# Performance work log

Hardware: AMD Instinct MI355X
Metric: run time of the kernel (lower is better)

## Reference

```python
import jax, jax.numpy as jnp
import numpy as np

STRIDE, PAD, DIL, DG = 1, 1, 1, 1
KH, KW = 3, 3


def setup_inputs() -> dict:
    key = jax.random.key(0)
    k1, k2, k3 = jax.random.split(key, 3)
    B, Cin, H, W, Cout = 8, 128, 64, 64, 256
    Ho = (H + 2 * PAD - (DIL * (KH - 1) + 1)) // STRIDE + 1
    Wo = (W + 2 * PAD - (DIL * (KW - 1) + 1)) // STRIDE + 1
    x = jax.random.normal(k1, (B, Cin, H, W), jnp.float32)
    offset = jax.random.normal(k2, (B, DG * 2 * KH * KW, Ho, Wo), jnp.float32)
    stdv = 1.0 / np.sqrt(Cin * KH * KW)
    weight = jax.random.uniform(k3, (Cout, Cin, KH, KW), jnp.float32, -stdv, stdv)
    return {"x": x, "offset": offset, "weight": weight}


def deform_conv2d(x, offset, weight, stride=STRIDE, pad=PAD, dil=DIL, dg=DG):
    """Deformable conv v1: per-tap learned offsets + bilinear gather + GEMM."""
    B, C, H, W = x.shape
    Co, Ci, kh, kw = weight.shape
    K = kh * kw
    cg = C // dg  # channels per deformable group
    Ho = (H + 2 * pad - (dil * (kh - 1) + 1)) // stride + 1
    Wo = (W + 2 * pad - (dil * (kw - 1) + 1)) // stride + 1

    # offset layout: [B, dg*K*2, Ho, Wo] with (dy, dx) interleaved per tap
    off = offset.reshape(B, dg, K, 2, Ho, Wo)

    # base sampling positions per output pixel and kernel tap
    ky, kx = jnp.meshgrid(jnp.arange(kh), jnp.arange(kw), indexing="ij")
    base_y = (jnp.arange(Ho) * stride - pad)[None, :, None] + (ky.reshape(K) * dil)[:, None, None]  # [K,Ho,1]
    base_x = (jnp.arange(Wo) * stride - pad)[None, None, :] + (kx.reshape(K) * dil)[:, None, None]  # [K,1,Wo]

    py = base_y[None, None].astype(offset.dtype) + off[:, :, :, 0]  # [B,dg,K,Ho,Wo]
    px = base_x[None, None].astype(offset.dtype) + off[:, :, :, 1]  # [B,dg,K,Ho,Wo]

    y0f = jnp.floor(py)
    x0f = jnp.floor(px)
    fy = py - y0f
    fx = px - x0f
    y0 = y0f.astype(jnp.int32)
    x0 = x0f.astype(jnp.int32)
    y1 = y0 + 1
    x1 = x0 + 1

    x_flat = x.reshape(B, dg, cg, H * W)

    def corner(yi, xi, w):
        # zero out contributions whose corner falls outside the image
        valid = (yi >= 0) & (yi < H) & (xi >= 0) & (xi < W)
        idx = jnp.clip(yi, 0, H - 1) * W + jnp.clip(xi, 0, W - 1)  # [B,dg,K,Ho,Wo]
        g = jax.vmap(jax.vmap(lambda xf, i: xf[:, i]))(x_flat, idx)  # [B,dg,cg,K,Ho,Wo]
        return g * (w * valid)[:, :, None]

    cols = (corner(y0, x0, (1 - fy) * (1 - fx))
            + corner(y0, x1, (1 - fy) * fx)
            + corner(y1, x0, fy * (1 - fx))
            + corner(y1, x1, fy * fx))  # [B,dg,cg,K,Ho,Wo]

    w_r = weight.reshape(Co, dg, cg, K)
    return jnp.einsum("bgckhw,ogck->bohw", cols, w_r)


def reference(x, offset, weight):
    return deform_conv2d(x, offset, weight)
```

## Files before the change

kernel.cpp:

```cpp
#include <hip/hip_runtime.h>
#include <hip/hip_bf16.h>

#define CIN   128
#define HH    64
#define WW    64
#define COUT  256
#define HO    64
#define WO    64
#define NTAP  9
#define KTOT  (CIN*NTAP)
#define BK    32
#define NSTEP (KTOT/BK)
#define NB    8
#define PXB   32
#define CROW  272

typedef __attribute__((ext_vector_type(8))) short bf16x8;
typedef __attribute__((ext_vector_type(4))) short bf16x4;
typedef __attribute__((ext_vector_type(4))) float f32x4;

struct __align__(16) TapEntry {
  int   i00, i01, i10, i11;
  float w00, w01, w10, w11;
};

static __device__ __forceinline__ ushort f2bf(float v) {
  unsigned u = __float_as_uint(v);
  unsigned rnd = 0x7fffu + ((u >> 16) & 1u);
  return (ushort)((u + rnd) >> 16);
}
static __device__ __forceinline__ float bf2f(short s) {
  return __uint_as_float(((unsigned)(unsigned short)s) << 16);
}

__global__ __launch_bounds__(256) void prep(const float* __restrict__ x,
                                            const float* __restrict__ w,
                                            ushort* __restrict__ xt,
                                            ushort* __restrict__ wbt) {
  const int blk = blockIdx.x;
  const int tid = threadIdx.x;
  if (blk < NB * HH) {
    const int b = blk >> 6, y = blk & 63;
    const int px = tid & 63, c8 = tid >> 6;
    const float* src = x + (size_t)b * CIN * HH * WW + y * WW + px;
    ushort* dst = xt + (((size_t)(b * HH + y) * WW) + px) * CIN;
    #pragma unroll
    for (int cc = 0; cc < 4; ++cc) {
      const int c0 = cc * 32 + c8 * 8;
      bf16x8 v;
      #pragma unroll
      for (int j = 0; j < 8; ++j)
        v[j] = (short)f2bf(src[(size_t)(c0 + j) * (HH * WW)]);
      *reinterpret_cast<bf16x8*>(dst + c0) = v;
    }
  } else {
    const int h = (blk - NB * HH) * 256 + tid;
    const int s   = h >> 10;
    const int c16 = (h >> 6) & 15;
    const int l   = h & 63;
    const int q   = l >> 4;
    const int r   = l & 15;
    const int co  = c16 * 16 + r;
    const int tap = s >> 2;
    const int ci0 = (s & 3) * 32 + q * 8;
    bf16x8 o;
    #pragma unroll
    for (int j = 0; j < 8; ++j)
      o[j] = (short)f2bf(w[(size_t)(co * CIN + ci0 + j) * NTAP + tap]);
    *reinterpret_cast<bf16x8*>(wbt + (size_t)h * 8) = o;
  }
}

__global__ __launch_bounds__(256, 4)
void dcn8(const ushort* __restrict__ xt, const float* __restrict__ off,
          const ushort* __restrict__ wbt, float* __restrict__ out)
{
  __shared__ TapEntry taps[NTAP * PXB];
  __shared__ __align__(16) char colsB[PXB * CROW];

  const int tid = threadIdx.x;
  const int b  = blockIdx.x & 7;
  const int ho = (blockIdx.x >> 3) & 63;
  const int ph = blockIdx.x >> 9;

  for (int e = tid; e < NTAP * PXB; e += 256) {
    const int k  = e >> 5;
    const int lw = e & 31;
    const int wo = ph * PXB + lw;
    const float* op = off + (((size_t)(b * 18 + 2 * k) * HO + ho) * WO + wo);
    const float dy = op[0];
    const float dx = op[HO * WO];
    const float py  = (float)(ho - 1 + (k / 3)) + dy;
    const float pxf = (float)(wo - 1 + (k % 3)) + dx;
    const float y0f = floorf(py), x0f = floorf(pxf);
    const float fy = py - y0f, fx = pxf - x0f;
    const int y0 = (int)y0f, x0 = (int)x0f;
    const int y1 = y0 + 1,  x1 = x0 + 1;
    const bool vy0 = (unsigned)y0 < HH, vy1 = (unsigned)y1 < HH;
    const bool vx0 = (unsigned)x0 < WW, vx1 = (unsigned)x1 < WW;
    const int cy0 = min(max(y0, 0), HH - 1), cy1 = min(max(y1, 0), HH - 1);
    const int cx0 = min(max(x0, 0), WW - 1), cx1 = min(max(x1, 0), WW - 1);
    TapEntry t;
    t.i00 = (cy0 * WW + cx0) << 8;  t.i01 = (cy0 * WW + cx1) << 8;
    t.i10 = (cy1 * WW + cx0) << 8;  t.i11 = (cy1 * WW + cx1) << 8;
    const float gy = 1.f - fy, gx = 1.f - fx;
    t.w00 = (vy0 && vx0) ? gy * gx : 0.f;
    t.w01 = (vy0 && vx1) ? gy * fx : 0.f;
    t.w10 = (vy1 && vx0) ? fy * gx : 0.f;
    t.w11 = (vy1 && vx1) ? fy * fx : 0.f;
    taps[e] = t;
  }

  const int lane = tid & 63;
  const int grp  = tid >> 6;
  const int l15  = lane & 15;
  const int q    = lane >> 4;
  const int s16b = l15 * 16;

  f32x4 acc[4][2];
  #pragma unroll
  for (int m = 0; m < 4; ++m)
    #pragma unroll
    for (int n = 0; n < 2; ++n)
      acc[m][n] = 0.f;

  const char* xb = reinterpret_cast<const char*>(xt)
                 + (size_t)b * (HH * WW * CIN * 2) + s16b;

  __syncthreads();

  #pragma unroll 1
  for (int tap = 0; tap < NTAP; ++tap) {
    const int px0 = (grp << 3) + q;
    const int px1 = (grp << 3) + 4 + q;
    const TapEntry te0 = taps[tap * PXB + px0];
    const TapEntry te1 = taps[tap * PXB + px1];
    const bf16x8 a00 = *reinterpret_cast<const bf16x8*>(xb + te0.i00);
    const bf16x8 a01 = *reinterpret_cast<const bf16x8*>(xb + te0.i01);
    const bf16x8 a10 = *reinterpret_cast<const bf16x8*>(xb + te0.i10);
    const bf16x8 a11 = *reinterpret_cast<const bf16x8*>(xb + te0.i11);
    const bf16x8 b00 = *reinterpret_cast<const bf16x8*>(xb + te1.i00);
    const bf16x8 b01 = *reinterpret_cast<const bf16x8*>(xb + te1.i01);
    const bf16x8 b10 = *reinterpret_cast<const bf16x8*>(xb + te1.i10);
    const bf16x8 b11 = *reinterpret_cast<const bf16x8*>(xb + te1.i11);
    bf16x8 h0, h1;
    #pragma unroll
    for (int j = 0; j < 8; ++j) {
      const float v0 = te0.w00 * bf2f(a00[j]) + te0.w01 * bf2f(a01[j])
                     + te0.w10 * bf2f(a10[j]) + te0.w11 * bf2f(a11[j]);
      h0[j] = (short)f2bf(v0);
      const float v1 = te1.w00 * bf2f(b00[j]) + te1.w01 * bf2f(b01[j])
                     + te1.w10 * bf2f(b10[j]) + te1.w11 * bf2f(b11[j]);
      h1[j] = (short)f2bf(v1);
    }

    __syncthreads();

    *reinterpret_cast<bf16x8*>(colsB + px0 * CROW + s16b) = h0;
    *reinterpret_cast<bf16x8*>(colsB + px1 * CROW + s16b) = h1;

    __syncthreads();

    #pragma unroll
    for (int kk = 0; kk < 4; ++kk) {
      const int s = tap * 4 + kk;
      bf16x8 a[4], bb[2];
      #pragma unroll
      for (int m = 0; m < 4; ++m)
        a[m] = *reinterpret_cast<const bf16x8*>(
            wbt + ((size_t)((s * 16 + grp * 4 + m) * 64 + lane)) * 8);
      #pragma unroll
      for (int n = 0; n < 2; ++n)
        bb[n] = *reinterpret_cast<const bf16x8*>(
            colsB + (n * 16 + l15) * CROW + kk * 64 + q * 16);
      #pragma unroll
      for (int m = 0; m < 4; ++m)
        #pragma unroll
        for (int n = 0; n < 2; ++n)
          acc[m][n] = __builtin_amdgcn_mfma_f32_16x16x32_bf16(
              a[m], bb[n], acc[m][n], 0, 0, 0);
    }
  }

  #pragma unroll
  for (int m = 0; m < 4; ++m)
    #pragma unroll
    for (int n = 0; n < 2; ++n)
      #pragma unroll
      for (int r = 0; r < 4; ++r) {
        const int co = grp * 64 + m * 16 + q * 4 + r;
        const int wo = ph * PXB + n * 16 + l15;
        out[(((size_t)b * COUT + co) * HO + ho) * WO + wo] = acc[m][n][r];
      }
}

__global__ __launch_bounds__(256, 2)
void dcn_f32(const float* __restrict__ x, const float* __restrict__ off,
             const float* __restrict__ wgt, float* __restrict__ out)
{
  __shared__ TapEntry taps[NTAP * WO];
  __shared__ __align__(16) ushort colsf[WO * 40];
  const int tid = threadIdx.x;
  const int b  = blockIdx.x & 7;
  const int ho = blockIdx.x >> 3;
  for (int e = tid; e < NTAP * WO; e += 256) {
    const int k  = e >> 6;
    const int wo = e & 63;
    const float* op = off + (((size_t)(b * 18 + 2 * k) * HO + ho) * WO + wo);
    const float dy = op[0];
    const float dx = op[HO * WO];
    const float py  = (float)(ho - 1 + (k / 3)) + dy;
    const float pxf = (float)(wo - 1 + (k % 3)) + dx;
    const float y0f = floorf(py), x0f = floorf(pxf);
    const float fy = py - y0f, fx = pxf - x0f;
    const int y0 = (int)y0f, x0 = (int)x0f;
    const int y1 = y0 + 1,  x1 = x0 + 1;
    const bool vy0 = (unsigned)y0 < HH, vy1 = (unsigned)y1 < HH;
    const bool vx0 = (unsigned)x0 < WW, vx1 = (unsigned)x1 < WW;
    const int cy0 = min(max(y0, 0), HH - 1), cy1 = min(max(y1, 0), HH - 1);
    const int cx0 = min(max(x0, 0), WW - 1), cx1 = min(max(x1, 0), WW - 1);
    TapEntry t;
    t.i00 = cy0 * WW + cx0; t.i01 = cy0 * WW + cx1;
    t.i10 = cy1 * WW + cx0; t.i11 = cy1 * WW + cx1;
    const float gy = 1.f - fy, gx = 1.f - fx;
    t.w00 = (vy0 && vx0) ? gy * gx : 0.f;
    t.w01 = (vy0 && vx1) ? gy * fx : 0.f;
    t.w10 = (vy1 && vx0) ? fy * gx : 0.f;
    t.w11 = (vy1 && vx1) ? fy * fx : 0.f;
    taps[e] = t;
  }
  const int px = tid & 63, grp = tid >> 6, lane = tid & 63;
  const int l15 = lane & 15, q = lane >> 4;
  f32x4 acc[4][4];
  #pragma unroll
  for (int m = 0; m < 4; ++m)
    #pragma unroll
    for (int n = 0; n < 4; ++n) acc[m][n] = 0.f;
  const float* xb = x + (size_t)b * CIN * HH * WW;
  __syncthreads();
  for (int tap = 0; tap < NTAP; ++tap) {
    const TapEntry e = taps[tap * WO + px];
    for (int cb = 0; cb < 4; ++cb) {
      __syncthreads();
      {
        const float* xp = xb + (size_t)(cb * 32 + grp * 8) * (HH * WW);
        bf16x8 hv;
        #pragma unroll
        for (int j = 0; j < 8; ++j) {
          const float* p = xp + j * (HH * WW);
          const float v = e.w00 * p[e.i00] + e.w01 * p[e.i01]
                        + e.w10 * p[e.i10] + e.w11 * p[e.i11];
          hv[j] = (short)f2bf(v);
        }
        *reinterpret_cast<bf16x8*>(
            reinterpret_cast<char*>(colsf) + px * 80 + grp * 16) = hv;
      }
      __syncthreads();
      bf16x8 a[4], bbf[4];
      #pragma unroll
      for (int m = 0; m < 4; ++m) {
        const int co = grp * 64 + m * 16 + l15;
        bf16x8 t;
        #pragma unroll
        for (int j = 0; j < 8; ++j)
          t[j] = (short)f2bf(wgt[(size_t)(co * CIN + cb * 32 + q * 8 + j) * NTAP + tap]);
        a[m] = t;
      }
      #pragma unroll
      for (int n = 0; n < 4; ++n)
        bbf[n] = *reinterpret_cast<const bf16x8*>(
            reinterpret_cast<const char*>(colsf) + (n * 16 + l15) * 80 + q * 16);
      #pragma unroll
      for (int m = 0; m < 4; ++m)
        #pragma unroll
        for (int n = 0; n < 4; ++n)
          acc[m][n] = __builtin_amdgcn_mfma_f32_16x16x32_bf16(
              a[m], bbf[n], acc[m][n], 0, 0, 0);
    }
  }
  const int wco = grp * 64;
  #pragma unroll
  for (int m = 0; m < 4; ++m)
    #pragma unroll
    for (int n = 0; n < 4; ++n)
      #pragma unroll
      for (int r = 0; r < 4; ++r) {
        const int co = wco + m * 16 + q * 4 + r;
        const int wo = n * 16 + l15;
        out[(((size_t)b * COUT + co) * HO + ho) * WO + wo] = acc[m][n][r];
      }
}

extern "C" void kernel_launch(void* const* d_in, const int* in_sizes, int n_in,
                              void* d_out, int out_size, void* d_ws, size_t ws_size,
                              hipStream_t stream) {
  const float* x   = (const float*)d_in[0];
  const float* off = (const float*)d_in[1];
  const float* wgt = (const float*)d_in[2];
  float* out = (float*)d_out;

  const size_t xt_bytes = (size_t)NB * HH * WW * CIN * sizeof(ushort);
  const size_t wb_bytes = (size_t)NSTEP * COUT * BK * sizeof(ushort);
  if (ws_size >= xt_bytes + wb_bytes) {
    ushort* xtp  = (ushort*)d_ws;
    ushort* wbtp = (ushort*)((char*)d_ws + xt_bytes);
    const int wchunks = NSTEP * COUT * BK / 8;
    const int wblocks = wchunks / 256;
    prep<<<NB * HH + wblocks, 256, 0, stream>>>(x, wgt, xtp, wbtp);
    dcn8<<<NB * HO * 2, 256, 0, stream>>>(xtp, off, wbtp, out);
  } else {
    dcn_f32<<<NB * HO, 256, 0, stream>>>(x, off, wgt, out);
  }
}
```

Before: 51.05 us.

## Double-buffer bilinear column tile and prefetch next tap's gathers during MFMA

The column tile in shared memory is now double-buffered. The gather loads for tap+1 are issued before the MFMA loop of the current tap, and the bilinear combine is written to the other buffer afterwards, so global gather latency overlaps with matrix math and one barrier per tap is removed. The bilinear combine is also rewritten with packed f32x2 math and a v_cvt_pk_bf16_f32 instruction in place of the scalar rounding routine. This costs more registers for the in-flight gathers and twice the LDS for the column tile, which could reduce occupancy.

```diff
diff --git a/kernel.cpp b/kernel.cpp
--- a/kernel.cpp
+++ b/kernel.cpp
@@ -14,10 +14,13 @@
 #define NB    8
 #define PXB   32
 #define CROW  272
+#define CBUF  (PXB*CROW)
 
 typedef __attribute__((ext_vector_type(8))) short bf16x8;
 typedef __attribute__((ext_vector_type(4))) short bf16x4;
 typedef __attribute__((ext_vector_type(4))) float f32x4;
+typedef __attribute__((ext_vector_type(2))) float f32x2;
+typedef __attribute__((ext_vector_type(4))) unsigned int u32x4;
 
 struct __align__(16) TapEntry {
   int   i00, i01, i10, i11;
@@ -31,6 +34,31 @@
 }
 static __device__ __forceinline__ float bf2f(short s) {
   return __uint_as_float(((unsigned)(unsigned short)s) << 16);
+}
+static __device__ __forceinline__ f32x2 unpack2(unsigned dw) {
+  f32x2 r;
+  r.x = __uint_as_float(dw << 16);
+  r.y = __uint_as_float(dw & 0xffff0000u);
+  return r;
+}
+
+static __device__ __forceinline__ u32x4 combine_pk(const u32x4 c00, const u32x4 c01,
+                                                   const u32x4 c10, const u32x4 c11,
+                                                   const float w00, const float w01,
+                                                   const float w10, const float w11) {
+  u32x4 out;
+  #pragma unroll
+  for (int d = 0; d < 4; ++d) {
+    f32x2 a;
+    a  = unpack2(c00[d]) * f32x2{w00, w00};
+    a += unpack2(c01[d]) * f32x2{w01, w01};
+    a += unpack2(c10[d]) * f32x2{w10, w10};
+    a += unpack2(c11[d]) * f32x2{w11, w11};
+    unsigned r;
+    asm("v_cvt_pk_bf16_f32 %0, %1, %2" : "=v"(r) : "v"(a.x), "v"(a.y));
+    out[d] = r;
+  }
+  return out;
 }
 
 __global__ __launch_bounds__(256) void prep(const float* __restrict__ x,
@@ -72,11 +100,11 @@
 }
 
 __global__ __launch_bounds__(256, 4)
-void dcn8(const ushort* __restrict__ xt, const float* __restrict__ off,
+void dcn9(const ushort* __restrict__ xt, const float* __restrict__ off,
           const ushort* __restrict__ wbt, float* __restrict__ out)
 {
   __shared__ TapEntry taps[NTAP * PXB];
-  __shared__ __align__(16) char colsB[PXB * CROW];
+  __shared__ __align__(16) char colsB[2 * CBUF];
 
   const int tid = threadIdx.x;
   const int b  = blockIdx.x & 7;
@@ -116,6 +144,8 @@
   const int l15  = lane & 15;
   const int q    = lane >> 4;
   const int s16b = l15 * 16;
+  const int px0  = (grp << 3) + q;
+  const int px1  = (grp << 3) + 4 + q;
 
   f32x4 acc[4][2];
   #pragma unroll
@@ -129,37 +159,47 @@
 
   __syncthreads();
 
+  {
+    const TapEntry t0 = taps[px0];
+    const TapEntry t1 = taps[px1];
+    const u32x4 a00 = *reinterpret_cast<const u32x4*>(xb + t0.i00);
+    const u32x4 a01 = *reinterpret_cast<const u32x4*>(xb + t0.i01);
+    const u32x4 a10 = *reinterpret_cast<const u32x4*>(xb + t0.i10);
+    const u32x4 a11 = *reinterpret_cast<const u32x4*>(xb + t0.i11);
+    const u32x4 b00 = *reinterpret_cast<const u32x4*>(xb + t1.i00);
+    const u32x4 b01 = *reinterpret_cast<const u32x4*>(xb + t1.i01);
+    const u32x4 b10 = *reinterpret_cast<const u32x4*>(xb + t1.i10);
+    const u32x4 b11 = *reinterpret_cast<const u32x4*>(xb + t1.i11);
+    const u32x4 h0 = combine_pk(a00, a01, a10, a11, t0.w00, t0.w01, t0.w10, t0.w11);
+    const u32x4 h1 = combine_pk(b00, b01, b10, b11, t1.w00, t1.w01, t1.w10, t1.w11);
+    *reinterpret_cast<u32x4*>(colsB + px0 * CROW + s16b) = h0;
+    *reinterpret_cast<u32x4*>(colsB + px1 * CROW + s16b) = h1;
+  }
+  __syncthreads();
+
   #pragma unroll 1
   for (int tap = 0; tap < NTAP; ++tap) {
-    const int px0 = (grp << 3) + q;
-    const int px1 = (grp << 3) + 4 + q;
-    const TapEntry te0 = taps[tap * PXB + px0];
-    const TapEntry te1 = taps[tap * PXB + px1];
-    const bf16x8 a00 = *reinterpret_cast<const bf16x8*>(xb + te0.i00);
-    const bf16x8 a01 = *reinterpret_cast<const bf16x8*>(xb + te0.i01);
-    const bf16x8 a10 = *reinterpret_cast<const bf16x8*>(xb + te0.i10);
-    const bf16x8 a11 = *reinterpret_cast<const bf16x8*>(xb + te0.i11);
-    const bf16x8 b00 = *reinterpret_cast<const bf16x8*>(xb + te1.i00);
-    const bf16x8 b01 = *reinterpret_cast<const bf16x8*>(xb + te1.i01);
-    const bf16x8 b10 = *reinterpret_cast<const bf16x8*>(xb + te1.i10);
-    const bf16x8 b11 = *reinterpret_cast<const bf16x8*>(xb + te1.i11);
-    bf16x8 h0, h1;
-    #pragma unroll
-    for (int j = 0; j < 8; ++j) {
-      const float v0 = te0.w00 * bf2f(a00[j]) + te0.w01 * bf2f(a01[j])
-                     + te0.w10 * bf2f(a10[j]) + te0.w11 * bf2f(a11[j]);
-      h0[j] = (short)f2bf(v0);
-      const float v1 = te1.w00 * bf2f(b00[j]) + te1.w01 * bf2f(b01[j])
-                     + te1.w10 * bf2f(b10[j]) + te1.w11 * bf2f(b11[j]);
-      h1[j] = (short)f2bf(v1);
-    }
-
-    __syncthreads();
-
-    *reinterpret_cast<bf16x8*>(colsB + px0 * CROW + s16b) = h0;
-    *reinterpret_cast<bf16x8*>(colsB + px1 * CROW + s16b) = h1;
-
-    __syncthreads();
+    const int  cur  = tap & 1;
+    const char* rbuf = colsB + cur * CBUF;
+    char*       wbuf = colsB + (cur ^ 1) * CBUF;
+    const bool  more = (tap + 1) < NTAP;
+
+    u32x4 a00, a01, a10, a11, b00, b01, b10, b11;
+    float w0a, w1a, w2a, w3a, w0b, w1b, w2b, w3b;
+    if (more) {
+      const TapEntry t0 = taps[(tap + 1) * PXB + px0];
+      const TapEntry t1 = taps[(tap + 1) * PXB + px1];
+      a00 = *reinterpret_cast<const u32x4*>(xb + t0.i00);
+      a01 = *reinterpret_cast<const u32x4*>(xb + t0.i01);
+      a10 = *reinterpret_cast<const u32x4*>(xb + t0.i10);
+      a11 = *reinterpret_cast<const u32x4*>(xb + t0.i11);
+      b00 = *reinterpret_cast<const u32x4*>(xb + t1.i00);
+      b01 = *reinterpret_cast<const u32x4*>(xb + t1.i01);
+      b10 = *reinterpret_cast<const u32x4*>(xb + t1.i10);
+      b11 = *reinterpret_cast<const u32x4*>(xb + t1.i11);
+      w0a = t0.w00; w1a = t0.w01; w2a = t0.w10; w3a = t0.w11;
+      w0b = t1.w00; w1b = t1.w01; w2b = t1.w10; w3b = t1.w11;
+    }
 
     #pragma unroll
     for (int kk = 0; kk < 4; ++kk) {
@@ -172,7 +212,7 @@
       #pragma unroll
       for (int n = 0; n < 2; ++n)
         bb[n] = *reinterpret_cast<const bf16x8*>(
-            colsB + (n * 16 + l15) * CROW + kk * 64 + q * 16);
+            rbuf + (n * 16 + l15) * CROW + kk * 64 + q * 16);
       #pragma unroll
       for (int m = 0; m < 4; ++m)
         #pragma unroll
@@ -180,6 +220,14 @@
           acc[m][n] = __builtin_amdgcn_mfma_f32_16x16x32_bf16(
               a[m], bb[n], acc[m][n], 0, 0, 0);
     }
+
+    if (more) {
+      const u32x4 h0 = combine_pk(a00, a01, a10, a11, w0a, w1a, w2a, w3a);
+      const u32x4 h1 = combine_pk(b00, b01, b10, b11, w0b, w1b, w2b, w3b);
+      *reinterpret_cast<u32x4*>(wbuf + px0 * CROW + s16b) = h0;
+      *reinterpret_cast<u32x4*>(wbuf + px1 * CROW + s16b) = h1;
+    }
+    __syncthreads();
   }
 
   #pragma unroll
@@ -307,7 +355,7 @@
     const int wchunks = NSTEP * COUT * BK / 8;
     const int wblocks = wchunks / 256;
     prep<<<NB * HH + wblocks, 256, 0, stream>>>(x, wgt, xtp, wbtp);
-    dcn8<<<NB * HO * 2, 256, 0, stream>>>(xtp, off, wbtp, out);
+    dcn9<<<NB * HO * 2, 256, 0, stream>>>(xtp, off, wbtp, out);
   } else {
     dcn_f32<<<NB * HO, 256, 0, stream>>>(x, off, wgt, out);
   }
```

Result: slower. 71.02 us (+39.1%).

## Process full output row per block with 512 threads and 32-channel warp tiles

Applied to the files above, without the earlier changes.

Merges the two half-row blocks into a single 512-thread block that covers all 64 output pixels of a row. Each of the 8 waves now owns 32 output channels across all 64 pixels instead of 64 channels across 32 pixels. The weight fragments loaded from global memory are shared across more pixels, which halves redundant weight traffic per output. The costs are a doubled shared-memory footprint, half as many blocks for scheduling, and more LDS reads of the column tile per wave.

```diff
diff --git a/kernel.cpp b/kernel.cpp
--- a/kernel.cpp
+++ b/kernel.cpp
@@ -12,7 +12,6 @@
 #define BK    32
 #define NSTEP (KTOT/BK)
 #define NB    8
-#define PXB   32
 #define CROW  272
 
 typedef __attribute__((ext_vector_type(8))) short bf16x8;
@@ -71,22 +70,20 @@
   }
 }
 
-__global__ __launch_bounds__(256, 4)
-void dcn8(const ushort* __restrict__ xt, const float* __restrict__ off,
-          const ushort* __restrict__ wbt, float* __restrict__ out)
+__global__ __launch_bounds__(512, 4)
+void dcn11(const ushort* __restrict__ xt, const float* __restrict__ off,
+           const ushort* __restrict__ wbt, float* __restrict__ out)
 {
-  __shared__ TapEntry taps[NTAP * PXB];
-  __shared__ __align__(16) char colsB[PXB * CROW];
+  __shared__ TapEntry taps[NTAP * WO];
+  __shared__ __align__(16) char colsB[WO * CROW];
 
   const int tid = threadIdx.x;
   const int b  = blockIdx.x & 7;
-  const int ho = (blockIdx.x >> 3) & 63;
-  const int ph = blockIdx.x >> 9;
-
-  for (int e = tid; e < NTAP * PXB; e += 256) {
-    const int k  = e >> 5;
-    const int lw = e & 31;
-    const int wo = ph * PXB + lw;
+  const int ho = blockIdx.x >> 3;
+
+  for (int e = tid; e < NTAP * WO; e += 512) {
+    const int k  = e >> 6;
+    const int wo = e & 63;
     const float* op = off + (((size_t)(b * 18 + 2 * k) * HO + ho) * WO + wo);
     const float dy = op[0];
     const float dx = op[HO * WO];
@@ -111,17 +108,19 @@
     taps[e] = t;
   }
 
+  const int wv   = tid >> 6;
   const int lane = tid & 63;
-  const int grp  = tid >> 6;
   const int l15  = lane & 15;
   const int q    = lane >> 4;
   const int s16b = l15 * 16;
-
-  f32x4 acc[4][2];
+  const int px0  = (wv << 3) + q;
+  const int px1  = (wv << 3) + 4 + q;
+
+  f32x4 acc[2][4];
   #pragma unroll
-  for (int m = 0; m < 4; ++m)
-    #pragma unroll
-    for (int n = 0; n < 2; ++n)
+  for (int m = 0; m < 2; ++m)
+    #pragma unroll
+    for (int n = 0; n < 4; ++n)
       acc[m][n] = 0.f;
 
   const char* xb = reinterpret_cast<const char*>(xt)
@@ -131,10 +130,8 @@
 
   #pragma unroll 1
   for (int tap = 0; tap < NTAP; ++tap) {
-    const int px0 = (grp << 3) + q;
-    const int px1 = (grp << 3) + 4 + q;
-    const TapEntry te0 = taps[tap * PXB + px0];
-    const TapEntry te1 = taps[tap * PXB + px1];
+    const TapEntry te0 = taps[tap * WO + px0];
+    const TapEntry te1 = taps[tap * WO + px1];
     const bf16x8 a00 = *reinterpret_cast<const bf16x8*>(xb + te0.i00);
     const bf16x8 a01 = *reinterpret_cast<const bf16x8*>(xb + te0.i01);
     const bf16x8 a10 = *reinterpret_cast<const bf16x8*>(xb + te0.i10);
@@ -164,32 +161,32 @@
     #pragma unroll
     for (int kk = 0; kk < 4; ++kk) {
       const int s = tap * 4 + kk;
-      bf16x8 a[4], bb[2];
-      #pragma unroll
-      for (int m = 0; m < 4; ++m)
+      bf16x8 a[2], bb[4];
+      #pragma unroll
+      for (int m = 0; m < 2; ++m)
         a[m] = *reinterpret_cast<const bf16x8*>(
-            wbt + ((size_t)((s * 16 + grp * 4 + m) * 64 + lane)) * 8);
-      #pragma unroll
-      for (int n = 0; n < 2; ++n)
+            wbt + ((size_t)((s * 16 + wv * 2 + m) * 64 + lane)) * 8);
+      #pragma unroll
+      for (int n = 0; n < 4; ++n)
         bb[n] = *reinterpret_cast<const bf16x8*>(
             colsB + (n * 16 + l15) * CROW + kk * 64 + q * 16);
       #pragma unroll
-      for (int m = 0; m < 4; ++m)
+      for (int m = 0; m < 2; ++m)
         #pragma unroll
-        for (int n = 0; n < 2; ++n)
+        for (int n = 0; n < 4; ++n)
           acc[m][n] = __builtin_amdgcn_mfma_f32_16x16x32_bf16(
               a[m], bb[n], acc[m][n], 0, 0, 0);
     }
   }
 
   #pragma unroll
-  for (int m = 0; m < 4; ++m)
-    #pragma unroll
-    for (int n = 0; n < 2; ++n)
+  for (int m = 0; m < 2; ++m)
+    #pragma unroll
+    for (int n = 0; n < 4; ++n)
       #pragma unroll
       for (int r = 0; r < 4; ++r) {
-        const int co = grp * 64 + m * 16 + q * 4 + r;
-        const int wo = ph * PXB + n * 16 + l15;
+        const int co = wv * 32 + m * 16 + q * 4 + r;
+        const int wo = n * 16 + l15;
         out[(((size_t)b * COUT + co) * HO + ho) * WO + wo] = acc[m][n][r];
       }
 }
@@ -307,7 +304,7 @@
     const int wchunks = NSTEP * COUT * BK / 8;
     const int wblocks = wchunks / 256;
     prep<<<NB * HH + wblocks, 256, 0, stream>>>(x, wgt, xtp, wbtp);
-    dcn8<<<NB * HO * 2, 256, 0, stream>>>(xtp, off, wbtp, out);
+    dcn11<<<NB * HO, 512, 0, stream>>>(xtp, off, wbtp, out);
   } else {
     dcn_f32<<<NB * HO, 256, 0, stream>>>(x, off, wgt, out);
   }
```

After: 57.24 us. +12.1%, slower.

## Prefetch bilinear corner gathers into LDS via global_load_lds one tap ahead

Applied to the files above, without the earlier changes.

Replaces the direct global loads of the four bilinear corners with asynchronous global-to-LDS loads into a per-wave staging buffer. The loads for the next tap are issued after the current tap's corners are consumed, so the gather latency overlaps the MFMA GEMM of the current tap. This adds 32KB of shared memory per block and lowers the launch-bounds occupancy hint from 4 to 2 blocks, which may reduce latency hiding across waves. The staging buffer is single-buffered, which relies on the vmcnt/lgkmcnt waits to keep reads and new writes ordered.

```diff
diff --git a/kernel.cpp b/kernel.cpp
--- a/kernel.cpp
+++ b/kernel.cpp
@@ -31,6 +31,12 @@
 }
 static __device__ __forceinline__ float bf2f(short s) {
   return __uint_as_float(((unsigned)(unsigned short)s) << 16);
+}
+
+static __device__ __forceinline__ void gload_lds16(const char* g, char* l) {
+  __builtin_amdgcn_global_load_lds(
+      (const __attribute__((address_space(1))) unsigned int*)g,
+      (__attribute__((address_space(3))) unsigned int*)l, 16, 0, 0);
 }
 
 __global__ __launch_bounds__(256) void prep(const float* __restrict__ x,
@@ -71,11 +77,12 @@
   }
 }
 
-__global__ __launch_bounds__(256, 4)
-void dcn8(const ushort* __restrict__ xt, const float* __restrict__ off,
-          const ushort* __restrict__ wbt, float* __restrict__ out)
+__global__ __launch_bounds__(256, 2)
+void dcn13(const ushort* __restrict__ xt, const float* __restrict__ off,
+           const ushort* __restrict__ wbt, float* __restrict__ out)
 {
   __shared__ TapEntry taps[NTAP * PXB];
+  __shared__ __align__(16) char stage[4 * 8 * 1024];
   __shared__ __align__(16) char colsB[PXB * CROW];
 
   const int tid = threadIdx.x;
@@ -116,6 +123,8 @@
   const int l15  = lane & 15;
   const int q    = lane >> 4;
   const int s16b = l15 * 16;
+  const int px0  = (grp << 3) + q;
+  const int px1  = (grp << 3) + 4 + q;
 
   f32x4 acc[4][2];
   #pragma unroll
@@ -126,23 +135,40 @@
 
   const char* xb = reinterpret_cast<const char*>(xt)
                  + (size_t)b * (HH * WW * CIN * 2) + s16b;
+  char* const stg = stage + grp * 8192;
 
   __syncthreads();
+
+  #define ISSUE_TAP(tap) do {                                         \
+    _Pragma("unroll")                                                  \
+    for (int h = 0; h < 2; ++h) {                                      \
+      const TapEntry te = taps[(tap) * PXB + (grp << 3) + (h << 2) + q]; \
+      char* sb = stg + h * 4096;                                       \
+      gload_lds16(xb + te.i00, sb);                                    \
+      gload_lds16(xb + te.i01, sb + 1024);                             \
+      gload_lds16(xb + te.i10, sb + 2048);                             \
+      gload_lds16(xb + te.i11, sb + 3072);                             \
+    }                                                                  \
+  } while (0)
+
+  ISSUE_TAP(0);
 
   #pragma unroll 1
   for (int tap = 0; tap < NTAP; ++tap) {
-    const int px0 = (grp << 3) + q;
-    const int px1 = (grp << 3) + 4 + q;
+    asm volatile("s_waitcnt vmcnt(0)" ::: "memory");
+    __builtin_amdgcn_sched_barrier(0);
+
+    const int rd = q * 256 + s16b;
+    const bf16x8 a00 = *reinterpret_cast<const bf16x8*>(stg + rd);
+    const bf16x8 a01 = *reinterpret_cast<const bf16x8*>(stg + 1024 + rd);
+    const bf16x8 a10 = *reinterpret_cast<const bf16x8*>(stg + 2048 + rd);
+    const bf16x8 a11 = *reinterpret_cast<const bf16x8*>(stg + 3072 + rd);
+    const bf16x8 b00 = *reinterpret_cast<const bf16x8*>(stg + 4096 + rd);
+    const bf16x8 b01 = *reinterpret_cast<const bf16x8*>(stg + 5120 + rd);
+    const bf16x8 b10 = *reinterpret_cast<const bf16x8*>(stg + 6144 + rd);
+    const bf16x8 b11 = *reinterpret_cast<const bf16x8*>(stg + 7168 + rd);
     const TapEntry te0 = taps[tap * PXB + px0];
     const TapEntry te1 = taps[tap * PXB + px1];
-    const bf16x8 a00 = *reinterpret_cast<const bf16x8*>(xb + te0.i00);
-    const bf16x8 a01 = *reinterpret_cast<const bf16x8*>(xb + te0.i01);
-    const bf16x8 a10 = *reinterpret_cast<const bf16x8*>(xb + te0.i10);
-    const bf16x8 a11 = *reinterpret_cast<const bf16x8*>(xb + te0.i11);
-    const bf16x8 b00 = *reinterpret_cast<const bf16x8*>(xb + te1.i00);
-    const bf16x8 b01 = *reinterpret_cast<const bf16x8*>(xb + te1.i01);
-    const bf16x8 b10 = *reinterpret_cast<const bf16x8*>(xb + te1.i10);
-    const bf16x8 b11 = *reinterpret_cast<const bf16x8*>(xb + te1.i11);
     bf16x8 h0, h1;
     #pragma unroll
     for (int j = 0; j < 8; ++j) {
@@ -154,6 +180,10 @@
       h1[j] = (short)f2bf(v1);
     }
 
+    asm volatile("s_waitcnt lgkmcnt(0)" ::: "memory");
+    __builtin_amdgcn_sched_barrier(0);
+    if (tap + 1 < NTAP) ISSUE_TAP(tap + 1);
+
     __syncthreads();
 
     *reinterpret_cast<bf16x8*>(colsB + px0 * CROW + s16b) = h0;
@@ -181,6 +211,7 @@
               a[m], bb[n], acc[m][n], 0, 0, 0);
     }
   }
+  #undef ISSUE_TAP
 
   #pragma unroll
   for (int m = 0; m < 4; ++m)
@@ -307,7 +338,7 @@
     const int wchunks = NSTEP * COUT * BK / 8;
     const int wblocks = wchunks / 256;
     prep<<<NB * HH + wblocks, 256, 0, stream>>>(x, wgt, xtp, wbtp);
-    dcn8<<<NB * HO * 2, 256, 0, stream>>>(xtp, off, wbtp, out);
+    dcn13<<<NB * HO * 2, 256, 0, stream>>>(xtp, off, wbtp, out);
   } else {
     dcn_f32<<<NB * HO, 256, 0, stream>>>(x, off, wgt, out);
   }
```

Measured after the change: 76.01 us. 48.9% more time.
